# Kernel optimization log

Measured on AMD Instinct MI355X. Metric: run time of the kernel, lower is better.

The kernel has to match this reference:

```python
import jax, jax.numpy as jnp
import numpy as np

B, S, C, HD = 2, 1024, 1024, 64
H = C // HD  # 16 heads
E = 4
EPS = 1e-5


def _ln(x, g, b):
    m = jnp.mean(x, axis=-1, keepdims=True)
    v = jnp.mean(jnp.square(x - m), axis=-1, keepdims=True)
    return (x - m) / jnp.sqrt(v + EPS) * g + b


def setup_inputs() -> dict:
    key = jax.random.key(0)
    ks = jax.random.split(key, 16)
    s = 0.02
    return {
        "fwd_x": jax.random.normal(ks[0], (B, S + 1, C), jnp.float32),
        "bwd_x": jax.random.normal(ks[1], (B, S + 1, C), jnp.float32),
        "pos_embed": jax.random.normal(ks[2], (S, HD), jnp.float32) * 0.01,
        "ln1_g": jnp.ones((C,), jnp.float32),
        "ln1_b": jnp.zeros((C,), jnp.float32),
        "Wq": jax.random.normal(ks[3], (C, C), jnp.float32) * s,
        "bq": jnp.zeros((C,), jnp.float32),
        "Wk": jax.random.normal(ks[4], (C, C), jnp.float32) * s,
        "bk": jnp.zeros((C,), jnp.float32),
        "Wv": jax.random.normal(ks[5], (C, C), jnp.float32) * s,
        "bv": jnp.zeros((C,), jnp.float32),
        "Wo": jax.random.normal(ks[6], (C, C), jnp.float32) * s,
        "bo": jnp.zeros((C,), jnp.float32),
        "ln2_g": jnp.ones((C,), jnp.float32),
        "ln2_b": jnp.zeros((C,), jnp.float32),
        "mlp_g": jnp.ones((C,), jnp.float32),
        "mlp_b": jnp.zeros((C,), jnp.float32),
        "W1": jax.random.normal(ks[7], (C, E * C), jnp.float32) * s,
        "b1": jnp.zeros((E * C,), jnp.float32),
        "W2": jax.random.normal(ks[8], (E * C, C), jnp.float32) * s,
        "b2": jnp.zeros((C,), jnp.float32),
    }


def reference(fwd_x, bwd_x, pos_embed, ln1_g, ln1_b, Wq, bq, Wk, bk, Wv, bv,
              Wo, bo, ln2_g, ln2_b, mlp_g, mlp_b, W1, b1, W2, b2):
    f = fwd_x[:, :-1, :]   # [B, S, C]
    r = bwd_x[:, 1:, :]    # [B, S, C]
    comb = (f + r) * np.float32(1.0 / np.sqrt(2.0))

    all_embed = jnp.concatenate([f, r], axis=1)       # [B, 2S, C]
    cx = _ln(comb, ln1_g, ln1_b)
    ae = _ln(all_embed, ln1_g, ln1_b)

    q = (cx @ Wq + bq).reshape(B, S, H, HD)
    k = (ae @ Wk + bk).reshape(B, 2 * S, H, HD)
    v = (ae @ Wv + bv).reshape(B, 2 * S, H, HD)

    pos2 = jnp.concatenate([pos_embed, pos_embed], axis=0)  # [2S, HD]
    k = k + pos2[None, :, None, :]
    q = (q + pos_embed[None, :, None, :]) * np.float32(1.0 / np.sqrt(HD))

    logits = jnp.einsum('bqhd,bkhd->bhqk', q, k)      # [B, H, S, 2S]

    qi = jnp.arange(S)[:, None]
    ki = jnp.arange(S)[None, :]
    l2r = ki <= qi   # causal (keys up to and incl. q) on first half
    r2l = ki >= qi   # anti-causal on second half
    mask = jnp.concatenate([l2r, r2l], axis=-1)        # [S, 2S]

    neg = jnp.finfo(logits.dtype).min
    attn = jax.nn.softmax(jnp.where(mask[None, None], logits, neg), axis=-1)

    o = jnp.einsum('bhqk,bkhd->bqhd', attn, v).reshape(B, S, C)
    o = o @ Wo + bo

    x = comb + o
    h = _ln(_ln(x, ln2_g, ln2_b), mlp_g, mlp_b)
    m = jax.nn.gelu(h @ W1 + b1, approximate=False) @ W2 + b2
    return x + m
```

## Files before the change

kernel.cpp:

```cpp
#include <hip/hip_runtime.h>
#include <hip/hip_bf16.h>
#include <cstdint>

#define DI __device__ __forceinline__

typedef unsigned short u16;
typedef __bf16 bf16x8 __attribute__((ext_vector_type(8)));
typedef float f32x4 __attribute__((ext_vector_type(4)));

constexpr int Bc  = 2;
constexpr int Sc  = 1024;
constexpr int Cc  = 1024;
constexpr int Hc  = 16;
constexpr int HDc = 64;
constexpr int S2c = 2048;
constexpr int ECc = 4096;
constexpr int BSc  = Bc * Sc;
constexpr int BS2c = Bc * S2c;

constexpr int EPI_KV = 0, EPI_Q = 1, EPI_O = 3, EPI_GELU = 4, EPI_FINAL = 5, EPI_PART = 6;

DI u16 f2b(float f) {
  __hip_bfloat16 h = __float2bfloat16(f);
  u16 u;
  __builtin_memcpy(&u, &h, 2);
  return u;
}

DI u16 f2b_fast(float f) {
  uint32_t u;
  __builtin_memcpy(&u, &f, 4);
  return (u16)((u + 0x8000u) >> 16);
}

DI void glds16(const void* g, void* l) {
  auto* lp = reinterpret_cast<__attribute__((address_space(3))) uint32_t*>(
      reinterpret_cast<uintptr_t>(l));
  __builtin_amdgcn_global_load_lds(
      reinterpret_cast<const __attribute__((address_space(1))) uint32_t*>(
          reinterpret_cast<uintptr_t>(g)),
      lp, 16, 0, 0);
}

DI f32x4 mfma16(bf16x8 a, bf16x8 b, f32x4 c) {
  return __builtin_amdgcn_mfma_f32_16x16x32_bf16(a, b, c, 0, 0, 0);
}

#define PIPE_WAIT(N)                                            \
  do {                                                          \
    asm volatile("s_waitcnt vmcnt(" #N ")" ::: "memory");       \
    __builtin_amdgcn_sched_barrier(0);                          \
  } while (0)
#define PIPE_BAR()                                              \
  do {                                                          \
    __builtin_amdgcn_s_barrier();                               \
    __builtin_amdgcn_sched_barrier(0);                          \
  } while (0)

__global__ __launch_bounds__(256) void transpose4_kernel(const float* __restrict__ Wq,
                                                         const float* __restrict__ Wk,
                                                         const float* __restrict__ Wv,
                                                         const float* __restrict__ Wo,
                                                         u16* __restrict__ WqT,
                                                         u16* __restrict__ WkvT,
                                                         u16* __restrict__ WoT) {
  __shared__ float tile[32][33];
  const int z = blockIdx.z;
  const float* W = (z == 0) ? Wq : (z == 1) ? Wk : (z == 2) ? Wv : Wo;
  u16* WT = (z == 0) ? WqT : (z == 1) ? WkvT : (z == 2) ? (WkvT + (size_t)Cc * Cc) : WoT;
  const int bx = blockIdx.x, by = blockIdx.y;
  const int tx = threadIdx.x, ty = threadIdx.y;
  const int c = bx * 32 + tx;
#pragma unroll
  for (int i = ty; i < 32; i += 8) tile[i][tx] = W[(size_t)(by * 32 + i) * Cc + c];
  __syncthreads();
#pragma unroll
  for (int i = ty; i < 32; i += 8)
    WT[(size_t)(bx * 32 + i) * Cc + by * 32 + tx] = f2b(tile[tx][i]);
}

__global__ __launch_bounds__(256) void transpose_kernel(const float* __restrict__ W,
                                                        u16* __restrict__ WT, int R, int Cn) {
  __shared__ float tile[32][33];
  const int bx = blockIdx.x, by = blockIdx.y;
  const int tx = threadIdx.x, ty = threadIdx.y;
  const int c = bx * 32 + tx;
#pragma unroll
  for (int i = ty; i < 32; i += 8) tile[i][tx] = W[(size_t)(by * 32 + i) * Cn + c];
  __syncthreads();
#pragma unroll
  for (int i = ty; i < 32; i += 8)
    WT[(size_t)(bx * 32 + i) * R + by * 32 + tx] = f2b(tile[tx][i]);
}

__global__ __launch_bounds__(256) void prep_ln_kernel(
    const float* __restrict__ fwd, const float* __restrict__ bwd, const float* __restrict__ g,
    const float* __restrict__ be, float* __restrict__ comb, u16* __restrict__ cx,
    u16* __restrict__ ae) {
  __shared__ float red[2][4];
  const int row = blockIdx.x, tid = threadIdx.x;
  const int c = tid * 4;
  float4 x;
  u16* dst;
  if (row < BSc) {
    const int b = row >> 10, s = row & (Sc - 1);
    const float4 f = *(const float4*)(fwd + ((size_t)(b * (Sc + 1) + s)) * Cc + c);
    const float4 r = *(const float4*)(bwd + ((size_t)(b * (Sc + 1) + s + 1)) * Cc + c);
    const float k = 0.70710678118654752f;
    x.x = (f.x + r.x) * k; x.y = (f.y + r.y) * k;
    x.z = (f.z + r.z) * k; x.w = (f.w + r.w) * k;
    *(float4*)(comb + (size_t)row * Cc + c) = x;
    dst = cx + (size_t)row * Cc;
  } else {
    const int idx = row - BSc;
    const int b = idx >> 11, t = idx & (S2c - 1);
    const float* src = (t < Sc) ? (fwd + ((size_t)(b * (Sc + 1) + t)) * Cc)
                                : (bwd + ((size_t)(b * (Sc + 1) + (t - Sc) + 1)) * Cc);
    x = *(const float4*)(src + c);
    dst = ae + (size_t)idx * Cc;
  }
  float s1 = x.x + x.y + x.z + x.w;
  float s2 = x.x * x.x + x.y * x.y + x.z * x.z + x.w * x.w;
  for (int off = 32; off; off >>= 1) { s1 += __shfl_down(s1, off); s2 += __shfl_down(s2, off); }
  if ((tid & 63) == 0) { red[0][tid >> 6] = s1; red[1][tid >> 6] = s2; }
  __syncthreads();
  s1 = red[0][0] + red[0][1] + red[0][2] + red[0][3];
  s2 = red[1][0] + red[1][1] + red[1][2] + red[1][3];
  const float mean = s1 * (1.0f / Cc);
  const float rstd = rsqrtf(s2 * (1.0f / Cc) - mean * mean + 1e-5f);
  const float4 gv = *(const float4*)(g + c);
  const float4 bv = *(const float4*)(be + c);
  ushort4 o;
  o.x = f2b((x.x - mean) * rstd * gv.x + bv.x);
  o.y = f2b((x.y - mean) * rstd * gv.y + bv.y);
  o.z = f2b((x.z - mean) * rstd * gv.z + bv.z);
  o.w = f2b((x.w - mean) * rstd * gv.w + bv.w);
  *(ushort4*)(dst + c) = o;
}

__global__ __launch_bounds__(256) void ln2_kernel(const float* __restrict__ x,
                                                  const float* __restrict__ g2,
                                                  const float* __restrict__ b2,
                                                  const float* __restrict__ gm,
                                                  const float* __restrict__ bm,
                                                  u16* __restrict__ h) {
  __shared__ float red[2][4];
  const int row = blockIdx.x, tid = threadIdx.x;
  const int c = tid * 4;
  const float4 v = *(const float4*)(x + (size_t)row * Cc + c);
  float s1 = v.x + v.y + v.z + v.w;
  float s2 = v.x * v.x + v.y * v.y + v.z * v.z + v.w * v.w;
  for (int off = 32; off; off >>= 1) { s1 += __shfl_down(s1, off); s2 += __shfl_down(s2, off); }
  if ((tid & 63) == 0) { red[0][tid >> 6] = s1; red[1][tid >> 6] = s2; }
  __syncthreads();
  s1 = red[0][0] + red[0][1] + red[0][2] + red[0][3];
  s2 = red[1][0] + red[1][1] + red[1][2] + red[1][3];
  float mean = s1 * (1.0f / Cc);
  float rstd = rsqrtf(s2 * (1.0f / Cc) - mean * mean + 1e-5f);
  const float4 ga = *(const float4*)(g2 + c);
  const float4 ba = *(const float4*)(b2 + c);
  const float t0 = (v.x - mean) * rstd * ga.x + ba.x;
  const float t1 = (v.y - mean) * rstd * ga.y + ba.y;
  const float t2 = (v.z - mean) * rstd * ga.z + ba.z;
  const float t3 = (v.w - mean) * rstd * ga.w + ba.w;
  s1 = t0 + t1 + t2 + t3;
  s2 = t0 * t0 + t1 * t1 + t2 * t2 + t3 * t3;
  for (int off = 32; off; off >>= 1) { s1 += __shfl_down(s1, off); s2 += __shfl_down(s2, off); }
  __syncthreads();
  if ((tid & 63) == 0) { red[0][tid >> 6] = s1; red[1][tid >> 6] = s2; }
  __syncthreads();
  s1 = red[0][0] + red[0][1] + red[0][2] + red[0][3];
  s2 = red[1][0] + red[1][1] + red[1][2] + red[1][3];
  mean = s1 * (1.0f / Cc);
  rstd = rsqrtf(s2 * (1.0f / Cc) - mean * mean + 1e-5f);
  const float4 gb = *(const float4*)(gm + c);
  const float4 bb = *(const float4*)(bm + c);
  ushort4 o;
  o.x = f2b((t0 - mean) * rstd * gb.x + bb.x);
  o.y = f2b((t1 - mean) * rstd * gb.y + bb.y);
  o.z = f2b((t2 - mean) * rstd * gb.z + bb.z);
  o.w = f2b((t3 - mean) * rstd * gb.w + bb.w);
  *(ushort4*)(h + (size_t)row * Cc + c) = o;
}

template <int EPI, int SK>
__global__ __launch_bounds__(256) void gemm_kernel(
    const u16* __restrict__ A, const u16* __restrict__ BT, const float* __restrict__ bias,
    const float* __restrict__ bias2, const float* __restrict__ pos,
    u16* __restrict__ outb, u16* __restrict__ out2, float* __restrict__ pbuf,
    int M, int N, int K) {
  __shared__ u16 A0s[128 * 32], A1s[128 * 32], A2s[128 * 32], A3s[128 * 32];
  __shared__ u16 B0s[128 * 32], B1s[128 * 32], B2s[128 * 32], B3s[128 * 32];
  const int tid = threadIdx.x;
  const int w = tid >> 6, lane = tid & 63, quad = lane >> 4, r16 = lane & 15;
  const int bm = blockIdx.y * 128, bn = blockIdx.x * 128;
  const int wm = (w & 1) * 64, wn = (w >> 1) * 64;
  const int Ks = K / SK, kb0 = blockIdx.z * Ks;

  const int srow = lane >> 2, scol = (lane & 3) * 8;
  const u16* aP = A + (size_t)(bm + w * 32 + srow) * K + kb0 + scol;
  const u16* bP = BT + (size_t)(bn + w * 32 + srow) * K + kb0 + scol;
  const size_t rstep = (size_t)16 * K;
  const int l0 = (w * 32) * 32;
  const int l1 = (w * 32 + 16) * 32;

  f32x4 acc[4][4] = {};

  auto STAGE = [&](u16* Ad, u16* Bd, int t) {
    const int ko = t * 32;
    glds16(aP + ko, Ad + l0);
    glds16(aP + ko + rstep, Ad + l1);
    glds16(bP + ko, Bd + l0);
    glds16(bP + ko + rstep, Bd + l1);
  };
  auto COMPUTE = [&](const u16* As, const u16* Bs) {
    bf16x8 af[4], bfr[4];
#pragma unroll
    for (int i = 0; i < 4; i++) {
      af[i] = *reinterpret_cast<const bf16x8*>(&As[(wm + i * 16 + r16) * 32 + quad * 8]);
      bfr[i] = *reinterpret_cast<const bf16x8*>(&Bs[(wn + i * 16 + r16) * 32 + quad * 8]);
    }
#pragma unroll
    for (int mi = 0; mi < 4; mi++)
#pragma unroll
      for (int ni = 0; ni < 4; ni++) acc[mi][ni] = mfma16(af[mi], bfr[ni], acc[mi][ni]);
  };

  const int NT = Ks / 32;
  STAGE(A0s, B0s, 0);
  STAGE(A1s, B1s, 1);
  for (int t = 0; t < NT; t += 4) {
    if (t + 2 < NT) { STAGE(A2s, B2s, t + 2); PIPE_WAIT(8); }
    else if (t + 1 < NT) PIPE_WAIT(4);
    else PIPE_WAIT(0);
    PIPE_BAR();
    COMPUTE(A0s, B0s);
    if (t + 3 < NT) { STAGE(A3s, B3s, t + 3); PIPE_WAIT(8); }
    else if (t + 2 < NT) PIPE_WAIT(4);
    else PIPE_WAIT(0);
    PIPE_BAR();
    COMPUTE(A1s, B1s);
    if (t + 4 < NT) { STAGE(A0s, B0s, t + 4); PIPE_WAIT(8); }
    else if (t + 3 < NT) PIPE_WAIT(4);
    else PIPE_WAIT(0);
    PIPE_BAR();
    COMPUTE(A2s, B2s);
    if (t + 5 < NT) { STAGE(A1s, B1s, t + 5); PIPE_WAIT(8); }
    else if (t + 4 < NT) PIPE_WAIT(4);
    else PIPE_WAIT(0);
    PIPE_BAR();
    COMPUTE(A3s, B3s);
  }

#pragma unroll
  for (int mi = 0; mi < 4; mi++) {
#pragma unroll
    for (int ni = 0; ni < 4; ni++) {
      const int col = bn + wn + ni * 16 + r16;
      const int row0 = bm + wm + mi * 16 + quad * 4;
      if constexpr (EPI == EPI_PART) {
        float* pb = pbuf + (size_t)blockIdx.z * M * N;
#pragma unroll
        for (int r = 0; r < 4; r++) pb[(size_t)(row0 + r) * N + col] = acc[mi][ni][r];
      } else if constexpr (EPI == EPI_KV) {
        if (col < Cc) {
#pragma unroll
          for (int r = 0; r < 4; r++) {
            const int row = row0 + r;
            const int key = row & (S2c - 1);
            const float y =
                acc[mi][ni][r] + bias[col] + pos[(key & (Sc - 1)) * HDc + (col & 63)];
            outb[(size_t)row * Cc + col] = f2b(y);
          }
        } else {
          const int c2 = col - Cc;
          const int h = c2 >> 6, d = c2 & 63;
          const int b = row0 >> 11, key0 = row0 & (S2c - 1);
          const float bb = bias2[c2];
          ushort4 pk;
          pk.x = f2b(acc[mi][ni][0] + bb);
          pk.y = f2b(acc[mi][ni][1] + bb);
          pk.z = f2b(acc[mi][ni][2] + bb);
          pk.w = f2b(acc[mi][ni][3] + bb);
          *(ushort4*)&out2[(((size_t)(b * Hc + h) * HDc + d) << 11) + key0] = pk;
        }
      } else {
#pragma unroll
        for (int r = 0; r < 4; r++) {
          const float y = acc[mi][ni][r] + bias[col];
          outb[(size_t)(row0 + r) * N + col] =
              f2b(0.5f * y * (1.0f + erff(y * 0.70710678118654752f)));
        }
      }
    }
  }
}

template <int EPI, int SK>
__global__ __launch_bounds__(256) void reduce_kernel(const float* __restrict__ pbuf,
                                                     const float* __restrict__ bias,
                                                     const float* __restrict__ pos,
                                                     const float* __restrict__ addsrc,
                                                     u16* __restrict__ outb,
                                                     float* __restrict__ outf, int M, int N) {
  const size_t flat = ((size_t)blockIdx.x * 256 + threadIdx.x) * 4;
  const int row = (int)(flat / N), col = (int)(flat % N);
  const size_t MN = (size_t)M * N;
  float4 s = *(const float4*)(pbuf + flat);
#pragma unroll
  for (int z = 1; z < SK; z++) {
    const float4 v = *(const float4*)(pbuf + z * MN + flat);
    s.x += v.x; s.y += v.y; s.z += v.z; s.w += v.w;
  }
  const float4 bv = *(const float4*)(bias + col);
  s.x += bv.x; s.y += bv.y; s.z += bv.z; s.w += bv.w;
  if constexpr (EPI == EPI_Q) {
    const int sq = row & (Sc - 1), d = col & 63;
    const float4 pv = *(const float4*)(pos + sq * HDc + d);
    constexpr float sc = 0.180336880111120426f;
    ushort4 o;
    o.x = f2b((s.x + pv.x) * sc);
    o.y = f2b((s.y + pv.y) * sc);
    o.z = f2b((s.z + pv.z) * sc);
    o.w = f2b((s.w + pv.w) * sc);
    *(ushort4*)(outb + flat) = o;
  } else {
    const float4 av = *(const float4*)(addsrc + flat);
    float4 o;
    o.x = s.x + av.x; o.y = s.y + av.y; o.z = s.z + av.z; o.w = s.w + av.w;
    *(float4*)(outf + flat) = o;
  }
}

__global__ __launch_bounds__(256) void attn_part_kernel(const u16* __restrict__ qb,
                                                        const u16* __restrict__ kb,
                                                        const u16* __restrict__ vT,
                                                        float* __restrict__ o_part,
                                                        float* __restrict__ l_part) {
  const int bh = blockIdx.x;
  const int qt = blockIdx.y;
  const int half = blockIdx.z;
  const int b = bh >> 4, head = bh & 15;
  const int tid = threadIdx.x;
  const int w = tid >> 6, lane = tid & 63, quad = lane >> 4, r16 = lane & 15;

  __shared__ u16 Kt[2][64 * 32];
  __shared__ u16 Vt[2][64 * 32];
  __shared__ u16 Ps[4][16 * 68];
  u16* ps = Ps[w];

  const int q0 = qt * 64;
  const int qw = q0 + w * 16;

  bf16x8 aq[2];
  {
    const u16* qp = qb + ((size_t)((b * Sc + qw + r16) * Hc + head)) * HDc + quad * 8;
    aq[0] = *(const bf16x8*)qp;
    aq[1] = *(const bf16x8*)(qp + 32);
  }

  const size_t krow = (size_t)Hc * HDc;
  const u16* kbase = kb + ((size_t)b * S2c * Hc + head) * HDc;
  const u16* vbase = vT + ((size_t)(b * Hc + head)) * HDc * S2c;

  const int srow = w * 16 + (lane >> 2);
  const int scol = (lane & 3) * 8;
  u16* kD0 = &Kt[0][w * 16 * 32];
  u16* kD1 = &Kt[1][w * 16 * 32];
  u16* vD0 = &Vt[0][w * 16 * 32];
  u16* vD1 = &Vt[1][w * 16 * 32];
  const u16* kS = kbase + (size_t)srow * krow + scol;
  const u16* vS = vbase + (size_t)srow * S2c + scol;

  f32x4 o_acc[4] = {};
  float lsum[4] = {};

  const int n = (half == 0) ? (qt + 1) : (16 - qt);
  const int kb0 = (half == 0) ? 0 : Sc + qt * 64;

  for (int j = 0; j < n; j++) {
    const int k0 = kb0 + j * 64;
    glds16(kS + (size_t)k0 * krow, kD0);
    glds16(kS + (size_t)k0 * krow + 32, kD1);
    glds16(vS + k0, vD0);
    glds16(vS + k0 + 32, vD1);
    __syncthreads();

    f32x4 sacc[4] = {};
#pragma unroll
    for (int ks = 0; ks < 2; ks++)
#pragma unroll
      for (int ni = 0; ni < 4; ni++) {
        const bf16x8 bk = *(const bf16x8*)&Kt[ks][(ni * 16 + r16) * 32 + quad * 8];
        sacc[ni] = mfma16(aq[ks], bk, sacc[ni]);
      }

    const int mode = (half == 0) ? ((j == n - 1) ? 1 : 0) : ((j == 0) ? 2 : 0);
#pragma unroll
    for (int r = 0; r < 4; r++) {
      const int qrow = qw + quad * 4 + r;
#pragma unroll
      for (int ni = 0; ni < 4; ni++) {
        float s = sacc[ni][r];
        if (mode == 1) { const int key = k0 + ni * 16 + r16; if (key > qrow) s = -128.0f; }
        else if (mode == 2) { const int key = k0 - Sc + ni * 16 + r16; if (key < qrow) s = -128.0f; }
        const float pe = __builtin_amdgcn_exp2f(s);
        lsum[r] += pe;
        ps[(quad * 4 + r) * 68 + ni * 16 + r16] = f2b_fast(pe);
      }
    }

#pragma unroll
    for (int ks = 0; ks < 2; ks++) {
      const bf16x8 ap = *(const bf16x8*)(&ps[r16 * 68 + ks * 32 + quad * 8]);
#pragma unroll
      for (int ni = 0; ni < 4; ni++) {
        const bf16x8 bv_ = *(const bf16x8*)&Vt[ks][(ni * 16 + r16) * 32 + quad * 8];
        o_acc[ni] = mfma16(ap, bv_, o_acc[ni]);
      }
    }
    __syncthreads();
  }

#pragma unroll
  for (int r = 0; r < 4; r++) {
    float l = lsum[r];
    l += __shfl_xor(l, 1);
    l += __shfl_xor(l, 2);
    l += __shfl_xor(l, 4);
    l += __shfl_xor(l, 8);
    lsum[r] = l;
  }

  const size_t rowbase = (((size_t)half * Bc + b) * Hc + head) * Sc + qw;
  float* ob = o_part + rowbase * HDc;
#pragma unroll
  for (int r = 0; r < 4; r++) {
    const int rl = quad * 4 + r;
#pragma unroll
    for (int ni = 0; ni < 4; ni++) ob[(size_t)rl * HDc + ni * 16 + r16] = o_acc[ni][r];
    if (r16 == 0) l_part[rowbase + rl] = lsum[r];
  }
}

__global__ __launch_bounds__(256) void attn_norm_kernel(const float* __restrict__ o_part,
                                                        const float* __restrict__ l_part,
                                                        u16* __restrict__ ob) {
  constexpr size_t HS = (size_t)Bc * Hc * Sc * HDc;
  constexpr size_t HL = (size_t)Bc * Hc * Sc;
  const int flat = blockIdx.x * 256 + threadIdx.x;
  const int row = flat >> 4, d0 = (flat & 15) * 4;
  const int q = row & (Sc - 1), h = (row >> 10) & 15, b = row >> 14;
  const float4 o0 = *(const float4*)(o_part + (size_t)row * HDc + d0);
  const float4 o1 = *(const float4*)(o_part + HS + (size_t)row * HDc + d0);
  const float rl = 1.0f / (l_part[row] + l_part[HL + row]);
  ushort4 o;
  o.x = f2b((o0.x + o1.x) * rl);
  o.y = f2b((o0.y + o1.y) * rl);
  o.z = f2b((o0.z + o1.z) * rl);
  o.w = f2b((o0.w + o1.w) * rl);
  *(ushort4*)(ob + ((size_t)((b * Sc + q) * Hc + h)) * HDc + d0) = o;
}

extern "C" void kernel_launch(void* const* d_in, const int* in_sizes, int n_in, void* d_out,
                              int out_size, void* d_ws, size_t ws_size, hipStream_t stream) {
  const float* fwd = (const float*)d_in[0];
  const float* bwd = (const float*)d_in[1];
  const float* pos = (const float*)d_in[2];
  const float* ln1g = (const float*)d_in[3];
  const float* ln1b = (const float*)d_in[4];
  const float* Wq = (const float*)d_in[5];
  const float* bq = (const float*)d_in[6];
  const float* Wk = (const float*)d_in[7];
  const float* bk = (const float*)d_in[8];
  const float* Wv = (const float*)d_in[9];
  const float* bv = (const float*)d_in[10];
  const float* Wo = (const float*)d_in[11];
  const float* bo = (const float*)d_in[12];
  const float* ln2g = (const float*)d_in[13];
  const float* ln2b = (const float*)d_in[14];
  const float* mlpg = (const float*)d_in[15];
  const float* mlpb = (const float*)d_in[16];
  const float* W1 = (const float*)d_in[17];
  const float* b1 = (const float*)d_in[18];
  const float* W2 = (const float*)d_in[19];
  const float* b2 = (const float*)d_in[20];

  char* p = (char*)d_ws;
  auto alloc = [&](size_t bytes) -> char* {
    char* r = p;
    p += (bytes + 255) & ~(size_t)255;
    return r;
  };
  float* comb = (float*)alloc((size_t)BSc * Cc * 4);
  float* xbuf = (float*)alloc((size_t)BSc * Cc * 4);
  u16* cx = (u16*)alloc((size_t)BSc * Cc * 2);
  u16* ae = (u16*)alloc((size_t)BS2c * Cc * 2);
  u16* qbuf = (u16*)alloc((size_t)BSc * Cc * 2);
  u16* kbuf = (u16*)alloc((size_t)BS2c * Cc * 2);
  u16* vTb = (u16*)alloc((size_t)BS2c * Cc * 2);
  u16* obuf = (u16*)alloc((size_t)BSc * Cc * 2);
  u16* hb = (u16*)alloc((size_t)BSc * Cc * 2);
  char* big = alloc((size_t)2 * BSc * Hc * HDc * 4 > (size_t)BSc * ECc * 2
                        ? (size_t)2 * BSc * Hc * HDc * 4
                        : (size_t)BSc * ECc * 2);
  float* o_part = (float*)big;
  u16* midb = (u16*)big;
  float* l_part = (float*)alloc((size_t)2 * Bc * Hc * Sc * 4);
  float* pbuf = (float*)alloc((size_t)4 * BSc * Cc * 4);
  u16* WqT = (u16*)alloc((size_t)Cc * Cc * 2);
  u16* WkvT = (u16*)alloc((size_t)2 * Cc * Cc * 2);
  u16* WoT = (u16*)alloc((size_t)Cc * Cc * 2);
  u16* W1T = (u16*)alloc((size_t)ECc * Cc * 2);
  u16* W2T = (u16*)alloc((size_t)Cc * ECc * 2);

  const dim3 tb(32, 8);
  transpose4_kernel<<<dim3(32, 32, 4), tb, 0, stream>>>(Wq, Wk, Wv, Wo, WqT, WkvT, WoT);
  transpose_kernel<<<dim3(128, 32), tb, 0, stream>>>(W1, W1T, Cc, ECc);
  transpose_kernel<<<dim3(32, 128), tb, 0, stream>>>(W2, W2T, ECc, Cc);

  prep_ln_kernel<<<BSc + BS2c, 256, 0, stream>>>(fwd, bwd, ln1g, ln1b, comb, cx, ae);

  gemm_kernel<EPI_PART, 4><<<dim3(Cc / 128, BSc / 128, 4), 256, 0, stream>>>(
      cx, WqT, nullptr, nullptr, nullptr, nullptr, nullptr, pbuf, BSc, Cc, Cc);
  reduce_kernel<EPI_Q, 4><<<(BSc * Cc / 4) / 256, 256, 0, stream>>>(
      pbuf, bq, pos, nullptr, qbuf, nullptr, BSc, Cc);

  gemm_kernel<EPI_KV, 1><<<dim3(2 * Cc / 128, BS2c / 128, 1), 256, 0, stream>>>(
      ae, WkvT, bk, bv, pos, kbuf, vTb, nullptr, BS2c, 2 * Cc, Cc);

  attn_part_kernel<<<dim3(Bc * Hc, Sc / 64, 2), 256, 0, stream>>>(qbuf, kbuf, vTb, o_part,
                                                                  l_part);
  attn_norm_kernel<<<(BSc * Hc * HDc / 4) / 256, 256, 0, stream>>>(o_part, l_part, obuf);

  gemm_kernel<EPI_PART, 4><<<dim3(Cc / 128, BSc / 128, 4), 256, 0, stream>>>(
      obuf, WoT, nullptr, nullptr, nullptr, nullptr, nullptr, pbuf, BSc, Cc, Cc);
  reduce_kernel<EPI_O, 4><<<(BSc * Cc / 4) / 256, 256, 0, stream>>>(
      pbuf, bo, nullptr, comb, nullptr, xbuf, BSc, Cc);

  ln2_kernel<<<BSc, 256, 0, stream>>>(xbuf, ln2g, ln2b, mlpg, mlpb, hb);

  gemm_kernel<EPI_GELU, 1><<<dim3(ECc / 128, BSc / 128, 1), 256, 0, stream>>>(
      hb, W1T, b1, nullptr, nullptr, midb, nullptr, nullptr, BSc, ECc, Cc);

  gemm_kernel<EPI_PART, 4><<<dim3(Cc / 128, BSc / 128, 4), 256, 0, stream>>>(
      midb, W2T, nullptr, nullptr, nullptr, nullptr, nullptr, pbuf, BSc, Cc, ECc);
  reduce_kernel<EPI_FINAL, 4><<<(BSc * Cc / 4) / 256, 256, 0, stream>>>(
      pbuf, b2, nullptr, xbuf, nullptr, (float*)d_out, BSc, Cc);
}
```

Baseline: 339.4 us.

## Merge attention halves into one block with 4-stage async K/V pipeline

Each query tile now walks all 17 of its key tiles (the causal part plus the anti-causal part) inside a single block, instead of launching two half-blocks and combining them in a separate normalization kernel. Normalization and the bf16 store are folded into the attention epilogue, which removes the fp32 partial O/l buffers and one kernel launch. K/V tiles stream through a 4-buffer shared-memory ring with async global-to-LDS loads issued two tiles ahead, so loads overlap MFMA work. In exchange there are half as many blocks (512) for the GPU to run in parallel, and LDS use per block grows.

```diff
diff --git a/kernel.cpp b/kernel.cpp
--- a/kernel.cpp
+++ b/kernel.cpp
@@ -332,25 +332,22 @@
   }
 }
 
-__global__ __launch_bounds__(256) void attn_part_kernel(const u16* __restrict__ qb,
-                                                        const u16* __restrict__ kb,
-                                                        const u16* __restrict__ vT,
-                                                        float* __restrict__ o_part,
-                                                        float* __restrict__ l_part) {
+__global__ __launch_bounds__(256) void attn_kernel(const u16* __restrict__ qb,
+                                                   const u16* __restrict__ kb,
+                                                   const u16* __restrict__ vT,
+                                                   u16* __restrict__ ob) {
   const int bh = blockIdx.x;
   const int qt = blockIdx.y;
-  const int half = blockIdx.z;
   const int b = bh >> 4, head = bh & 15;
   const int tid = threadIdx.x;
   const int w = tid >> 6, lane = tid & 63, quad = lane >> 4, r16 = lane & 15;
 
-  __shared__ u16 Kt[2][64 * 32];
-  __shared__ u16 Vt[2][64 * 32];
+  __shared__ u16 K0s[4096], K1s[4096], K2s[4096], K3s[4096];
+  __shared__ u16 V0s[4096], V1s[4096], V2s[4096], V3s[4096];
   __shared__ u16 Ps[4][16 * 68];
   u16* ps = Ps[w];
 
-  const int q0 = qt * 64;
-  const int qw = q0 + w * 16;
+  const int qw = qt * 64 + w * 16;
 
   bf16x8 aq[2];
   {
@@ -365,37 +362,34 @@
 
   const int srow = w * 16 + (lane >> 2);
   const int scol = (lane & 3) * 8;
-  u16* kD0 = &Kt[0][w * 16 * 32];
-  u16* kD1 = &Kt[1][w * 16 * 32];
-  u16* vD0 = &Vt[0][w * 16 * 32];
-  u16* vD1 = &Vt[1][w * 16 * 32];
+  const int stg = w * 16 * 32;
   const u16* kS = kbase + (size_t)srow * krow + scol;
   const u16* vS = vbase + (size_t)srow * S2c + scol;
 
   f32x4 o_acc[4] = {};
   float lsum[4] = {};
 
-  const int n = (half == 0) ? (qt + 1) : (16 - qt);
-  const int kb0 = (half == 0) ? 0 : Sc + qt * 64;
-
-  for (int j = 0; j < n; j++) {
-    const int k0 = kb0 + j * 64;
-    glds16(kS + (size_t)k0 * krow, kD0);
-    glds16(kS + (size_t)k0 * krow + 32, kD1);
-    glds16(vS + k0, vD0);
-    glds16(vS + k0 + 32, vD1);
-    __syncthreads();
-
+  auto K0OF = [&](int p) -> int { return (p <= qt) ? p * 64 : Sc + (p - 1) * 64; };
+
+  auto STAGE = [&](u16* Kd, u16* Vd, int p) {
+    const int k0 = K0OF(p);
+    glds16(kS + (size_t)k0 * krow, Kd + stg);
+    glds16(kS + (size_t)k0 * krow + 32, Kd + 2048 + stg);
+    glds16(vS + k0, Vd + stg);
+    glds16(vS + k0 + 32, Vd + 2048 + stg);
+  };
+
+  auto COMPUTE = [&](const u16* Kc, const u16* Vc, int p) {
+    const int k0 = K0OF(p);
     f32x4 sacc[4] = {};
 #pragma unroll
     for (int ks = 0; ks < 2; ks++)
 #pragma unroll
       for (int ni = 0; ni < 4; ni++) {
-        const bf16x8 bk = *(const bf16x8*)&Kt[ks][(ni * 16 + r16) * 32 + quad * 8];
+        const bf16x8 bk = *(const bf16x8*)&Kc[ks * 2048 + (ni * 16 + r16) * 32 + quad * 8];
         sacc[ni] = mfma16(aq[ks], bk, sacc[ni]);
       }
-
-    const int mode = (half == 0) ? ((j == n - 1) ? 1 : 0) : ((j == 0) ? 2 : 0);
+    const int mode = (p == qt) ? 1 : ((p == qt + 1) ? 2 : 0);
 #pragma unroll
     for (int r = 0; r < 4; r++) {
       const int qrow = qw + quad * 4 + r;
@@ -409,17 +403,49 @@
         ps[(quad * 4 + r) * 68 + ni * 16 + r16] = f2b_fast(pe);
       }
     }
-
 #pragma unroll
     for (int ks = 0; ks < 2; ks++) {
       const bf16x8 ap = *(const bf16x8*)(&ps[r16 * 68 + ks * 32 + quad * 8]);
 #pragma unroll
       for (int ni = 0; ni < 4; ni++) {
-        const bf16x8 bv_ = *(const bf16x8*)&Vt[ks][(ni * 16 + r16) * 32 + quad * 8];
+        const bf16x8 bv_ = *(const bf16x8*)&Vc[ks * 2048 + (ni * 16 + r16) * 32 + quad * 8];
         o_acc[ni] = mfma16(ap, bv_, o_acc[ni]);
       }
     }
-    __syncthreads();
+  };
+
+  constexpr int NU = 17;
+  STAGE(K0s, V0s, 0);
+  STAGE(K1s, V1s, 1);
+  for (int t = 0; t < NU; t += 4) {
+    {
+      if (t + 2 < NU) { STAGE(K2s, V2s, t + 2); PIPE_WAIT(8); }
+      else if (t + 1 < NU) PIPE_WAIT(4);
+      else PIPE_WAIT(0);
+      PIPE_BAR();
+      COMPUTE(K0s, V0s, t);
+    }
+    if (t + 1 < NU) {
+      if (t + 3 < NU) { STAGE(K3s, V3s, t + 3); PIPE_WAIT(8); }
+      else if (t + 2 < NU) PIPE_WAIT(4);
+      else PIPE_WAIT(0);
+      PIPE_BAR();
+      COMPUTE(K1s, V1s, t + 1);
+    }
+    if (t + 2 < NU) {
+      if (t + 4 < NU) { STAGE(K0s, V0s, t + 4); PIPE_WAIT(8); }
+      else if (t + 3 < NU) PIPE_WAIT(4);
+      else PIPE_WAIT(0);
+      PIPE_BAR();
+      COMPUTE(K2s, V2s, t + 2);
+    }
+    if (t + 3 < NU) {
+      if (t + 5 < NU) { STAGE(K1s, V1s, t + 5); PIPE_WAIT(8); }
+      else if (t + 4 < NU) PIPE_WAIT(4);
+      else PIPE_WAIT(0);
+      PIPE_BAR();
+      COMPUTE(K3s, V3s, t + 3);
+    }
   }
 
 #pragma unroll
@@ -429,37 +455,14 @@
     l += __shfl_xor(l, 2);
     l += __shfl_xor(l, 4);
     l += __shfl_xor(l, 8);
-    lsum[r] = l;
-  }
-
-  const size_t rowbase = (((size_t)half * Bc + b) * Hc + head) * Sc + qw;
-  float* ob = o_part + rowbase * HDc;
+    lsum[r] = 1.0f / l;
+  }
 #pragma unroll
   for (int r = 0; r < 4; r++) {
-    const int rl = quad * 4 + r;
-#pragma unroll
-    for (int ni = 0; ni < 4; ni++) ob[(size_t)rl * HDc + ni * 16 + r16] = o_acc[ni][r];
-    if (r16 == 0) l_part[rowbase + rl] = lsum[r];
-  }
-}
-
-__global__ __launch_bounds__(256) void attn_norm_kernel(const float* __restrict__ o_part,
-                                                        const float* __restrict__ l_part,
-                                                        u16* __restrict__ ob) {
-  constexpr size_t HS = (size_t)Bc * Hc * Sc * HDc;
-  constexpr size_t HL = (size_t)Bc * Hc * Sc;
-  const int flat = blockIdx.x * 256 + threadIdx.x;
-  const int row = flat >> 4, d0 = (flat & 15) * 4;
-  const int q = row & (Sc - 1), h = (row >> 10) & 15, b = row >> 14;
-  const float4 o0 = *(const float4*)(o_part + (size_t)row * HDc + d0);
-  const float4 o1 = *(const float4*)(o_part + HS + (size_t)row * HDc + d0);
-  const float rl = 1.0f / (l_part[row] + l_part[HL + row]);
-  ushort4 o;
-  o.x = f2b((o0.x + o1.x) * rl);
-  o.y = f2b((o0.y + o1.y) * rl);
-  o.z = f2b((o0.z + o1.z) * rl);
-  o.w = f2b((o0.w + o1.w) * rl);
-  *(ushort4*)(ob + ((size_t)((b * Sc + q) * Hc + h)) * HDc + d0) = o;
+    u16* od = ob + ((size_t)((b * Sc + qw + quad * 4 + r) * Hc + head)) * HDc;
+#pragma unroll
+    for (int ni = 0; ni < 4; ni++) od[ni * 16 + r16] = f2b(o_acc[ni][r] * lsum[r]);
+  }
 }
 
 extern "C" void kernel_launch(void* const* d_in, const int* in_sizes, int n_in, void* d_out,
@@ -501,12 +504,7 @@
   u16* vTb = (u16*)alloc((size_t)BS2c * Cc * 2);
   u16* obuf = (u16*)alloc((size_t)BSc * Cc * 2);
   u16* hb = (u16*)alloc((size_t)BSc * Cc * 2);
-  char* big = alloc((size_t)2 * BSc * Hc * HDc * 4 > (size_t)BSc * ECc * 2
-                        ? (size_t)2 * BSc * Hc * HDc * 4
-                        : (size_t)BSc * ECc * 2);
-  float* o_part = (float*)big;
-  u16* midb = (u16*)big;
-  float* l_part = (float*)alloc((size_t)2 * Bc * Hc * Sc * 4);
+  u16* midb = (u16*)alloc((size_t)BSc * ECc * 2);
   float* pbuf = (float*)alloc((size_t)4 * BSc * Cc * 4);
   u16* WqT = (u16*)alloc((size_t)Cc * Cc * 2);
   u16* WkvT = (u16*)alloc((size_t)2 * Cc * Cc * 2);
@@ -529,9 +527,7 @@
   gemm_kernel<EPI_KV, 1><<<dim3(2 * Cc / 128, BS2c / 128, 1), 256, 0, stream>>>(
       ae, WkvT, bk, bv, pos, kbuf, vTb, nullptr, BS2c, 2 * Cc, Cc);
 
-  attn_part_kernel<<<dim3(Bc * Hc, Sc / 64, 2), 256, 0, stream>>>(qbuf, kbuf, vTb, o_part,
-                                                                  l_part);
-  attn_norm_kernel<<<(BSc * Hc * HDc / 4) / 256, 256, 0, stream>>>(o_part, l_part, obuf);
+  attn_kernel<<<dim3(Bc * Hc, Sc / 64), 256, 0, stream>>>(qbuf, kbuf, vTb, obuf);
 
   gemm_kernel<EPI_PART, 4><<<dim3(Cc / 128, BSc / 128, 4), 256, 0, stream>>>(
       obuf, WoT, nullptr, nullptr, nullptr, nullptr, nullptr, pbuf, BSc, Cc, Cc);
```

After: 331.9 us. -2.2%, faster.
